# Kernel optimization log

Hardware: AMD Instinct MI355X
Metric: run time of the kernel (lower is better)

Reference implementation:

```python
import jax, jax.numpy as jnp
import numpy as np


def setup_inputs() -> dict:
    key = jax.random.key(0)
    k1, k2 = jax.random.split(key)
    B, N, M, D = 8, 8192, 8192, 3
    x = jax.random.normal(k1, (B, N, D), dtype=jnp.float32)
    y = jax.random.normal(k2, (B, M, D), dtype=jnp.float32)
    return {"x": x, "y": y}


def reference(x, y):
    # dist[b, i, j] = |x_bi|^2 + |y_bj|^2 - 2 * <x_bi, y_bj>
    # (same math as the torch code's rx.transpose(2,1) + ry - 2*xy, but
    #  computed with row-norm vectors instead of full NxN / MxM bmms)
    xx = jnp.sum(x * x, axis=-1)                      # [B, N]
    yy = jnp.sum(y * y, axis=-1)                      # [B, M]
    xy = jnp.einsum('bnd,bmd->bnm', x, y)             # [B, N, M]
    dist = xx[:, :, None] + yy[:, None, :] - 2.0 * xy # [B, N, M]
    dist1 = jnp.min(dist, axis=1)  # min over x points -> per-y nearest  [B, M]
    dist2 = jnp.min(dist, axis=2)  # min over y points -> per-x nearest  [B, N]
    return jnp.mean(dist1) + jnp.mean(dist2)
```

## Files before the change

### kernel.cpp

```cpp
#include <hip/hip_runtime.h>


#define B_ 8
#define N_ 8192
#define PTS (B_ * N_)
#define TPB 512

typedef short bf16x8 __attribute__((ext_vector_type(8)));
typedef float f32x16 __attribute__((ext_vector_type(16)));

__device__ __forceinline__ unsigned b16(float f) {
  unsigned u = __float_as_uint(f);
  return (u + 0x7FFFu + ((u >> 16) & 1u)) >> 16;
}
__device__ __forceinline__ float bf(unsigned h) { return __uint_as_float(h << 16); }

__device__ __forceinline__ void build_chunk(const float* __restrict__ cb,
                                            uint4* __restrict__ dst, int t) {
  const unsigned one = 0x3F80u;
#pragma unroll
  for (int q = 0; q < 2; ++q) {
    int p = t + q * TPB;
    float c0 = cb[3 * p], c1 = cb[3 * p + 1], c2 = cb[3 * p + 2];
    float nc = fmaf(c0, c0, fmaf(c1, c1, c2 * c2));
    unsigned yh0 = b16(c0), yh1 = b16(c1), yh2 = b16(c2);
    unsigned yl0 = b16(c0 - bf(yh0)), yl1 = b16(c1 - bf(yh1)), yl2 = b16(c2 - bf(yh2));
    unsigned nh = b16(nc), nl = b16(nc - bf(nh));
    int tt = p >> 5, mm = p & 31;
    dst[tt * 64 + mm]      = make_uint4(yh0 | (yh1 << 16), yh2 | (yl0 << 16),
                                        yl1 | (yl2 << 16), yh0 | (yh1 << 16));
    dst[tt * 64 + 32 + mm] = make_uint4(yh2 | (one << 16), one | (nh << 16),
                                        nl, 0u);
  }
}

__global__ __launch_bounds__(TPB, 4) void chamfer_main_k(
    const float* __restrict__ x, const float* __restrict__ y,
    float* __restrict__ gpart) {
  __shared__ uint4 ldsFrag[2][32 * 64];

  const unsigned one = 0x3F80u;
  int t = threadIdx.x, lane = t & 63, w = t >> 6;
  int b = blockIdx.x;
  int g = b >> 1;
  int hf = b & 1;
  int dir = g >> 7;
  int gg = g & 127;
  int batch = gg >> 4;
  int seg = gg & 15;
  const float* __restrict__ own  = dir ? y : x;
  const float* __restrict__ cand = dir ? x : y;

  int m = lane & 31;
  int rowBase = batch * N_ + seg * 512 + w * 64;
  bf16x8 A0, A1;
#pragma unroll
  for (int a = 0; a < 2; ++a) {
    const float* po = own + 3 * (rowBase + a * 32 + m);
    float v0 = po[0], v1 = po[1], v2 = po[2];
    float nv = fmaf(v0, v0, fmaf(v1, v1, v2 * v2));
    float a0 = -2.0f * v0, a1 = -2.0f * v1, a2 = -2.0f * v2;
    unsigned ah0 = b16(a0), ah1 = b16(a1), ah2 = b16(a2);
    unsigned al0 = b16(a0 - bf(ah0)), al1 = b16(a1 - bf(ah1)), al2 = b16(a2 - bf(ah2));
    unsigned nh = b16(nv), nl = b16(nv - bf(nh));
    uint4 h0 = make_uint4(ah0 | (ah1 << 16), ah2 | (ah0 << 16),
                          ah1 | (ah2 << 16), al0 | (al1 << 16));
    uint4 h1 = make_uint4(al2 | (nh << 16), nl | (one << 16), one, 0u);
    uint4 afr;
    afr.x = (lane < 32) ? h0.x : h1.x;
    afr.y = (lane < 32) ? h0.y : h1.y;
    afr.z = (lane < 32) ? h0.z : h1.z;
    afr.w = (lane < 32) ? h0.w : h1.w;
    if (a == 0) A0 = __builtin_bit_cast(bf16x8, afr);
    else        A1 = __builtin_bit_cast(bf16x8, afr);
  }

  f32x16 z = {0.f,0.f,0.f,0.f,0.f,0.f,0.f,0.f,0.f,0.f,0.f,0.f,0.f,0.f,0.f,0.f};
  f32x16 rm0, rm1;
#pragma unroll
  for (int r = 0; r < 16; ++r) { rm0[r] = 1e30f; rm1[r] = 1e30f; }

  const float* cbb = cand + (batch * N_ + hf * 4096) * 3;
  build_chunk(cbb, ldsFrag[0], t);
  __syncthreads();

  for (int ch = 0; ch < 4; ++ch) {
    const uint4* cur = ldsFrag[ch & 1];
    if (ch < 3)
      build_chunk(cbb + (ch + 1) * 1024 * 3, ldsFrag[(ch + 1) & 1], t);

#pragma unroll 2
    for (int i = 0; i < 16; ++i) {
      bf16x8 B0 = __builtin_bit_cast(bf16x8, cur[(2 * i) * 64 + lane]);
      bf16x8 B1 = __builtin_bit_cast(bf16x8, cur[(2 * i + 1) * 64 + lane]);
      f32x16 acc0 = __builtin_amdgcn_mfma_f32_32x32x16_bf16(A0, B0, z, 0, 0, 0);
      f32x16 acc1 = __builtin_amdgcn_mfma_f32_32x32x16_bf16(A1, B0, z, 0, 0, 0);
      f32x16 acc2 = __builtin_amdgcn_mfma_f32_32x32x16_bf16(A0, B1, z, 0, 0, 0);
      f32x16 acc3 = __builtin_amdgcn_mfma_f32_32x32x16_bf16(A1, B1, z, 0, 0, 0);
#pragma unroll
      for (int r = 0; r < 16; ++r) {
        rm0[r] = fminf(fminf(rm0[r], acc0[r]), acc2[r]);
        rm1[r] = fminf(fminf(rm1[r], acc1[r]), acc3[r]);
      }
    }
    __syncthreads();
  }

#pragma unroll
  for (int msk = 1; msk <= 16; msk <<= 1)
#pragma unroll
    for (int r = 0; r < 16; ++r) {
      rm0[r] = fminf(rm0[r], __shfl_xor(rm0[r], msk, 64));
      rm1[r] = fminf(rm1[r], __shfl_xor(rm1[r], msk, 64));
    }

  float* gp = gpart + b * 512;
  if ((lane & 31) == 0) {
    int h = lane >> 5;
#pragma unroll
    for (int r = 0; r < 16; ++r) {
      int rr = (r & 3) + 8 * (r >> 2) + 4 * h;
      gp[w * 64 + rr] = rm0[r];
      gp[w * 64 + 32 + rr] = rm1[r];
    }
  }
}

__global__ __launch_bounds__(256) void chamfer_final_k(
    const float* __restrict__ gpart, float* __restrict__ out) {
  int i = blockIdx.x * 256 + threadIdx.x;
  float s = 0.0f;
#pragma unroll
  for (int e = 0; e < 4; ++e) {
    int rowid = 4 * i + e;
    int g = rowid >> 9, r = rowid & 511;
    s += fminf(gpart[(2 * g) * 512 + r], gpart[(2 * g + 1) * 512 + r]);
  }
  for (int off = 32; off > 0; off >>= 1) s += __shfl_down(s, off, 64);
  __shared__ float red[4];
  int lane = threadIdx.x & 63, wv = threadIdx.x >> 6;
  if (lane == 0) red[wv] = s;
  __syncthreads();
  if (threadIdx.x == 0) {
    float tt = (red[0] + red[1]) + (red[2] + red[3]);
    atomicAdd(out, tt * (1.0f / (float)PTS));
  }
}

extern "C" void kernel_launch(void* const* d_in, const int* in_sizes, int n_in,
                              void* d_out, int out_size, void* d_ws, size_t ws_size,
                              hipStream_t stream) {
  const float* x = (const float*)d_in[0];
  const float* y = (const float*)d_in[1];
  float* out = (float*)d_out;
  float* gpart = (float*)d_ws;

  hipMemsetAsync(out, 0, sizeof(float), stream);
  chamfer_main_k<<<512, TPB, 0, stream>>>(x, y, gpart);
  chamfer_final_k<<<128, 256, 0, stream>>>(gpart, out);
}
```

Before: 94.07 us.

## Precompute bf16 MFMA fragments in a prepass kernel and stream them into LDS

Adds a preprocessing kernel that converts x and y once into split-bf16 A and B fragment layouts stored in workspace. The main kernel then loads ready fragments directly instead of recomputing the hi/lo bf16 split per block, which was redundant across the 16 segments per batch. Candidate chunks are staged through registers and written to LDS after the compute loop, and B fragments are prefetched from LDS one iteration ahead. The cost is an extra kernel launch plus workspace writes and reads of about 8 MB, and an extra barrier per chunk.

```diff
diff --git a/kernel.cpp b/kernel.cpp
--- a/kernel.cpp
+++ b/kernel.cpp
@@ -15,31 +15,45 @@
 }
 __device__ __forceinline__ float bf(unsigned h) { return __uint_as_float(h << 16); }
 
-__device__ __forceinline__ void build_chunk(const float* __restrict__ cb,
-                                            uint4* __restrict__ dst, int t) {
+__global__ __launch_bounds__(256) void chamfer_pre_k(
+    const float* __restrict__ x, const float* __restrict__ y,
+    uint4* __restrict__ afX, uint4* __restrict__ bfX,
+    uint4* __restrict__ afY, uint4* __restrict__ bfY,
+    float* __restrict__ out) {
+  int p = blockIdx.x * 256 + threadIdx.x;
+  if (p == 0) out[0] = 0.0f;
   const unsigned one = 0x3F80u;
+  int tile = p >> 5, m = p & 31;
+  int i0 = tile * 64 + m, i1 = tile * 64 + 32 + m;
+
 #pragma unroll
-  for (int q = 0; q < 2; ++q) {
-    int p = t + q * TPB;
-    float c0 = cb[3 * p], c1 = cb[3 * p + 1], c2 = cb[3 * p + 2];
-    float nc = fmaf(c0, c0, fmaf(c1, c1, c2 * c2));
-    unsigned yh0 = b16(c0), yh1 = b16(c1), yh2 = b16(c2);
-    unsigned yl0 = b16(c0 - bf(yh0)), yl1 = b16(c1 - bf(yh1)), yl2 = b16(c2 - bf(yh2));
-    unsigned nh = b16(nc), nl = b16(nc - bf(nh));
-    int tt = p >> 5, mm = p & 31;
-    dst[tt * 64 + mm]      = make_uint4(yh0 | (yh1 << 16), yh2 | (yl0 << 16),
-                                        yl1 | (yl2 << 16), yh0 | (yh1 << 16));
-    dst[tt * 64 + 32 + mm] = make_uint4(yh2 | (one << 16), one | (nh << 16),
-                                        nl, 0u);
+  for (int s = 0; s < 2; ++s) {
+    const float* src = s ? y : x;
+    uint4* af = s ? afY : afX;
+    uint4* bf_ = s ? bfY : bfX;
+    float v0 = src[3 * p], v1 = src[3 * p + 1], v2 = src[3 * p + 2];
+    float nv = fmaf(v0, v0, fmaf(v1, v1, v2 * v2));
+    unsigned nh = b16(nv), nl = b16(nv - bf(nh));
+    float a0 = -2.0f * v0, a1 = -2.0f * v1, a2 = -2.0f * v2;
+    unsigned ah0 = b16(a0), ah1 = b16(a1), ah2 = b16(a2);
+    unsigned al0 = b16(a0 - bf(ah0)), al1 = b16(a1 - bf(ah1)), al2 = b16(a2 - bf(ah2));
+    af[i0] = make_uint4(ah0 | (ah1 << 16), ah2 | (ah0 << 16),
+                        ah1 | (ah2 << 16), al0 | (al1 << 16));
+    af[i1] = make_uint4(al2 | (nh << 16), nl | (one << 16), one, 0u);
+    unsigned yh0 = b16(v0), yh1 = b16(v1), yh2 = b16(v2);
+    unsigned yl0 = b16(v0 - bf(yh0)), yl1 = b16(v1 - bf(yh1)), yl2 = b16(v2 - bf(yh2));
+    bf_[i0] = make_uint4(yh0 | (yh1 << 16), yh2 | (yl0 << 16),
+                         yl1 | (yl2 << 16), yh0 | (yh1 << 16));
+    bf_[i1] = make_uint4(yh2 | (one << 16), one | (nh << 16), nl, 0u);
   }
 }
 
 __global__ __launch_bounds__(TPB, 4) void chamfer_main_k(
-    const float* __restrict__ x, const float* __restrict__ y,
+    const uint4* __restrict__ afX, const uint4* __restrict__ bfX,
+    const uint4* __restrict__ afY, const uint4* __restrict__ bfY,
     float* __restrict__ gpart) {
   __shared__ uint4 ldsFrag[2][32 * 64];
 
-  const unsigned one = 0x3F80u;
   int t = threadIdx.x, lane = t & 63, w = t >> 6;
   int b = blockIdx.x;
   int g = b >> 1;
@@ -48,62 +62,59 @@
   int gg = g & 127;
   int batch = gg >> 4;
   int seg = gg & 15;
-  const float* __restrict__ own  = dir ? y : x;
-  const float* __restrict__ cand = dir ? x : y;
+  const uint4* __restrict__ arow = dir ? afY : afX;
+  const uint4* __restrict__ bcand = dir ? bfX : bfY;
 
-  int m = lane & 31;
-  int rowBase = batch * N_ + seg * 512 + w * 64;
-  bf16x8 A0, A1;
-#pragma unroll
-  for (int a = 0; a < 2; ++a) {
-    const float* po = own + 3 * (rowBase + a * 32 + m);
-    float v0 = po[0], v1 = po[1], v2 = po[2];
-    float nv = fmaf(v0, v0, fmaf(v1, v1, v2 * v2));
-    float a0 = -2.0f * v0, a1 = -2.0f * v1, a2 = -2.0f * v2;
-    unsigned ah0 = b16(a0), ah1 = b16(a1), ah2 = b16(a2);
-    unsigned al0 = b16(a0 - bf(ah0)), al1 = b16(a1 - bf(ah1)), al2 = b16(a2 - bf(ah2));
-    unsigned nh = b16(nv), nl = b16(nv - bf(nh));
-    uint4 h0 = make_uint4(ah0 | (ah1 << 16), ah2 | (ah0 << 16),
-                          ah1 | (ah2 << 16), al0 | (al1 << 16));
-    uint4 h1 = make_uint4(al2 | (nh << 16), nl | (one << 16), one, 0u);
-    uint4 afr;
-    afr.x = (lane < 32) ? h0.x : h1.x;
-    afr.y = (lane < 32) ? h0.y : h1.y;
-    afr.z = (lane < 32) ? h0.z : h1.z;
-    afr.w = (lane < 32) ? h0.w : h1.w;
-    if (a == 0) A0 = __builtin_bit_cast(bf16x8, afr);
-    else        A1 = __builtin_bit_cast(bf16x8, afr);
-  }
+  int tb = batch * 256 + seg * 16 + w * 2;
+  bf16x8 A0 = __builtin_bit_cast(bf16x8, arow[tb * 64 + lane]);
+  bf16x8 A1 = __builtin_bit_cast(bf16x8, arow[(tb + 1) * 64 + lane]);
 
   f32x16 z = {0.f,0.f,0.f,0.f,0.f,0.f,0.f,0.f,0.f,0.f,0.f,0.f,0.f,0.f,0.f,0.f};
   f32x16 rm0, rm1;
 #pragma unroll
   for (int r = 0; r < 16; ++r) { rm0[r] = 1e30f; rm1[r] = 1e30f; }
 
-  const float* cbb = cand + (batch * N_ + hf * 4096) * 3;
-  build_chunk(cbb, ldsFrag[0], t);
+  const uint4* __restrict__ cb = bcand + (batch * 256 + hf * 128) * 64;
+  uint4 stg[4];
+#pragma unroll
+  for (int k = 0; k < 4; ++k) stg[k] = cb[t + k * TPB];
+#pragma unroll
+  for (int k = 0; k < 4; ++k) ldsFrag[0][t + k * TPB] = stg[k];
   __syncthreads();
 
   for (int ch = 0; ch < 4; ++ch) {
     const uint4* cur = ldsFrag[ch & 1];
-    if (ch < 3)
-      build_chunk(cbb + (ch + 1) * 1024 * 3, ldsFrag[(ch + 1) & 1], t);
+    if (ch < 3) {
+      const uint4* nxt = cb + (ch + 1) * 2048;
+#pragma unroll
+      for (int k = 0; k < 4; ++k) stg[k] = nxt[t + k * TPB];
+    }
 
-#pragma unroll 2
+    uint4 b0 = cur[lane], b1 = cur[64 + lane];
     for (int i = 0; i < 16; ++i) {
-      bf16x8 B0 = __builtin_bit_cast(bf16x8, cur[(2 * i) * 64 + lane]);
-      bf16x8 B1 = __builtin_bit_cast(bf16x8, cur[(2 * i + 1) * 64 + lane]);
-      f32x16 acc0 = __builtin_amdgcn_mfma_f32_32x32x16_bf16(A0, B0, z, 0, 0, 0);
-      f32x16 acc1 = __builtin_amdgcn_mfma_f32_32x32x16_bf16(A1, B0, z, 0, 0, 0);
-      f32x16 acc2 = __builtin_amdgcn_mfma_f32_32x32x16_bf16(A0, B1, z, 0, 0, 0);
-      f32x16 acc3 = __builtin_amdgcn_mfma_f32_32x32x16_bf16(A1, B1, z, 0, 0, 0);
+      uint4 nb0, nb1;
+      if (i < 15) { nb0 = cur[(2 * i + 2) * 64 + lane]; nb1 = cur[(2 * i + 3) * 64 + lane]; }
+      bf16x8 Bt0 = __builtin_bit_cast(bf16x8, b0);
+      bf16x8 Bt1 = __builtin_bit_cast(bf16x8, b1);
+      f32x16 acc0 = __builtin_amdgcn_mfma_f32_32x32x16_bf16(A0, Bt0, z, 0, 0, 0);
+      f32x16 acc1 = __builtin_amdgcn_mfma_f32_32x32x16_bf16(A0, Bt1, z, 0, 0, 0);
+      f32x16 acc2 = __builtin_amdgcn_mfma_f32_32x32x16_bf16(A1, Bt0, z, 0, 0, 0);
+      f32x16 acc3 = __builtin_amdgcn_mfma_f32_32x32x16_bf16(A1, Bt1, z, 0, 0, 0);
 #pragma unroll
       for (int r = 0; r < 16; ++r) {
-        rm0[r] = fminf(fminf(rm0[r], acc0[r]), acc2[r]);
-        rm1[r] = fminf(fminf(rm1[r], acc1[r]), acc3[r]);
+        rm0[r] = fminf(fminf(rm0[r], acc0[r]), acc1[r]);
+        rm1[r] = fminf(fminf(rm1[r], acc2[r]), acc3[r]);
       }
+      b0 = nb0; b1 = nb1;
     }
+
     __syncthreads();
+    if (ch < 3) {
+      uint4* nbuf = ldsFrag[(ch + 1) & 1];
+#pragma unroll
+      for (int k = 0; k < 4; ++k) nbuf[t + k * TPB] = stg[k];
+      __syncthreads();
+    }
   }
 
 #pragma unroll
@@ -153,9 +164,14 @@
   const float* x = (const float*)d_in[0];
   const float* y = (const float*)d_in[1];
   float* out = (float*)d_out;
-  float* gpart = (float*)d_ws;
+  uint4* afX = (uint4*)d_ws;
+  uint4* bfX = afX + 2048 * 64;
+  uint4* afY = bfX + 2048 * 64;
+  uint4* bfY = afY + 2048 * 64;
+  float* gpart = (float*)(bfY + 2048 * 64);
 
   hipMemsetAsync(out, 0, sizeof(float), stream);
-  chamfer_main_k<<<512, TPB, 0, stream>>>(x, y, gpart);
+  chamfer_pre_k<<<PTS / 256, 256, 0, stream>>>(x, y, afX, bfX, afY, bfY, out);
+  chamfer_main_k<<<512, TPB, 0, stream>>>(afX, bfX, afY, bfY, gpart);
   chamfer_final_k<<<128, 256, 0, stream>>>(gpart, out);
 }
```

Measured after the change: 110.0 us. +17.0%, slower.
